# Optimization experiments

Measured on AMD Instinct MI355X. Metric: run time of the kernel, lower is better.

Reference implementation:

```python
import jax, jax.numpy as jnp
import numpy as np

# ---- static hash-grid config (matches tcnn HashGrid in __init__) ----
L = 16            # n_levels
T = 1 << 19       # hashmap size per level
BASE = 16
MAXR = 4096
GEO = 15
SCALE = np.exp((np.log(MAXR) - np.log(BASE)) / (L - 1))
RES = np.floor(BASE * SCALE ** np.arange(L)).astype(np.int64)  # per-level resolution
PRIMES = np.array([1, 2654435761, 805459861], dtype=np.uint32)
CORNERS = np.array([[(i >> 2) & 1, (i >> 1) & 1, i & 1] for i in range(8)], dtype=np.float32)  # [8,3]


@jax.custom_vjp
def trunc_exp(x):
    return jnp.exp(x)

def _te_fwd(x):
    return jnp.exp(x), x

def _te_bwd(x, g):
    return (g * jnp.exp(jnp.minimum(x, 15.0)),)

trunc_exp.defvjp(_te_fwd, _te_bwd)


def hash_encode(x, tables):
    """Multi-res hash grid. x: [N,3] in [0,1]; tables: [L,T,2] -> [N, 2*L]."""
    x = jnp.clip(x, 0.0, 1.0)
    feats = []
    for l in range(L):  # fixed small loop over levels
        res = float(RES[l])
        pos = x * res                      # [N,3]
        p0 = jnp.floor(pos)
        f = pos - p0                       # trilinear fractions
        idx = (p0[:, None, :] + CORNERS[None]).astype(jnp.uint32)  # [N,8,3]
        h = (idx[..., 0] * PRIMES[0]) ^ (idx[..., 1] * PRIMES[1]) ^ (idx[..., 2] * PRIMES[2])
        h = (h % np.uint32(T)).astype(jnp.int32)                   # [N,8]
        w = jnp.prod(jnp.where(CORNERS[None] > 0, f[:, None, :], 1.0 - f[:, None, :]), axis=-1)  # [N,8]
        feats.append(jnp.sum(tables[l][h] * w[..., None], axis=1))  # [N,2]
    return jnp.concatenate(feats, axis=-1)  # [N,32]


def sh_deg4(d):
    """Spherical harmonics degree 4 (16 comps) on unit directions d: [N,3]."""
    x, y, z = d[..., 0], d[..., 1], d[..., 2]
    x2, y2, z2 = x * x, y * y, z * z
    xy, yz, xz = x * y, y * z, x * z
    return jnp.stack([
        jnp.full_like(x, 0.28209479177387814),
        -0.48860251190291987 * y, 0.48860251190291987 * z, -0.48860251190291987 * x,
        1.0925484305920792 * xy, -1.0925484305920792 * yz,
        0.94617469575755997 * z2 - 0.31539156525252005,
        -1.0925484305920792 * xz, 0.54627421529603959 * (x2 - y2),
        -0.5900435899266435 * y * (3 * x2 - y2), 2.890611442640554 * xy * z,
        -0.4570457994644658 * y * (4 * z2 - x2 - y2),
        0.3731763325901154 * z * (2 * z2 - 3 * x2 - 3 * y2),
        -0.4570457994644658 * x * (4 * z2 - x2 - y2),
        1.445305721320277 * z * (x2 - y2),
        -0.5900435899266435 * x * (x2 - 3 * y2),
    ], axis=-1)


def setup_inputs() -> dict:
    key = jax.random.key(0)
    ks = jax.random.split(key, 12)
    R, N = 8192, 524288
    rays_o = jax.random.uniform(ks[0], (R, 3), minval=-0.4, maxval=0.4, dtype=jnp.float32)
    d = jax.random.normal(ks[1], (R, 3), dtype=jnp.float32)
    rays_d = d / jnp.linalg.norm(d, axis=-1, keepdims=True)
    ray_indices = jnp.sort(jax.random.randint(ks[2], (N,), 0, R)).astype(jnp.int32)
    t_starts = jax.random.uniform(ks[3], (N,), dtype=jnp.float32) * 0.25
    t_ends = t_starts + jax.random.uniform(ks[4], (N,), dtype=jnp.float32) * 0.02 + 1e-3
    hash_tables = jax.random.uniform(ks[5], (L, T, 2), minval=-1e-4, maxval=1e-4, dtype=jnp.float32)
    base_w0 = jax.random.normal(ks[6], (32, 64), dtype=jnp.float32) * (1.0 / np.sqrt(32))
    base_w1 = jax.random.normal(ks[7], (64, 16), dtype=jnp.float32) * (1.0 / np.sqrt(64))
    head_w0 = jax.random.normal(ks[8], (31, 64), dtype=jnp.float32) * (1.0 / np.sqrt(31))
    head_w1 = jax.random.normal(ks[9], (64, 64), dtype=jnp.float32) * (1.0 / np.sqrt(64))
    head_w2 = jax.random.normal(ks[10], (64, 3), dtype=jnp.float32) * (1.0 / np.sqrt(64))
    aabb = jnp.array([-1., -1., -1., 1., 1., 1.], dtype=jnp.float32)
    return dict(t_starts=t_starts, t_ends=t_ends, rays_o=rays_o, rays_d=rays_d,
                ray_indices=ray_indices, hash_tables=hash_tables,
                base_w0=base_w0, base_w1=base_w1,
                head_w0=head_w0, head_w1=head_w1, head_w2=head_w2, aabb=aabb)


def reference(t_starts, t_ends, rays_o, rays_d, ray_indices, hash_tables,
              base_w0, base_w1, head_w0, head_w1, head_w2, aabb):
    n_rays = rays_o.shape[0]
    aabb_min, aabb_max = aabb[:3], aabb[3:]
    # gather per-sample origins/dirs (irregular gather)
    t_origins = rays_o[ray_indices]
    t_dirs = rays_d[ray_indices]
    tmid = (t_starts + t_ends) * 0.5
    positions = t_origins + t_dirs * tmid[:, None]
    # query_density
    xn = (positions - aabb_min) / (aabb_max - aabb_min + 1e-5)
    selector = jnp.all((xn > 0.0) & (xn < 1.0), axis=-1)
    enc = hash_encode(xn, hash_tables)                   # [N,32]
    h = jax.nn.relu(enc @ base_w0) @ base_w1             # [N,16]
    sigmas = trunc_exp(h[:, 0] - 1.0) * selector         # [N]
    embedding = h[:, 1:]                                 # [N,15]
    # query_rgb: dir=(dir+1)/2 then SH enc maps back to [-1,1] => SH(t_dirs)
    hh = jnp.concatenate([sh_deg4(t_dirs), embedding], axis=-1)  # [N,31]
    rgbs = jax.nn.sigmoid(jax.nn.relu(jax.nn.relu(hh @ head_w0) @ head_w1) @ head_w2)  # [N,3]
    # render_weight_from_density: segment-wise exclusive transmittance
    s = sigmas * (t_ends - t_starts)
    excl = jnp.cumsum(s) - s                              # global exclusive cumsum
    offsets = jax.ops.segment_min(excl, ray_indices, num_segments=n_rays)  # value at each segment start
    trans = jnp.exp(-(excl - offsets[ray_indices]))
    alphas = 1.0 - jnp.exp(-s)
    weights = trans * alphas
    # accumulate_along_rays (segment_sum scatter)
    colors = jax.ops.segment_sum(weights[:, None] * rgbs, ray_indices, num_segments=n_rays)
    opacities = jax.ops.segment_sum(weights, ray_indices, num_segments=n_rays)[:, None]
    depths = jax.ops.segment_sum(weights * tmid, ray_indices, num_segments=n_rays)[:, None]
    depths = depths / jnp.maximum(opacities, jnp.finfo(jnp.float32).eps)  # expected_depths
    return colors, opacities, depths
```

## Files before the change

kernel.cpp:

```cpp
#include <hip/hip_runtime.h>
#include <math.h>

#define NLEV 16
#define TBL  (1u << 19)
#define TMASK (TBL - 1u)

typedef _Float16 half2v  __attribute__((ext_vector_type(2)));
typedef _Float16 half4   __attribute__((ext_vector_type(4)));
typedef _Float16 half8   __attribute__((ext_vector_type(8)));
typedef float    floatx4 __attribute__((ext_vector_type(4)));
typedef unsigned int uint4v __attribute__((ext_vector_type(4)));

struct ResParams { float resf[NLEV]; };

__device__ __forceinline__ float sigmoidf(float x) {
    return 1.0f / (1.0f + __expf(-x));
}

__device__ __forceinline__ int swz64(int row, int col) {
    return row * 64 + ((((col >> 3) ^ (row & 7)) << 3) | (col & 7));
}
__device__ __forceinline__ int swz64_blk(int row, int blk) {
    return row * 64 + ((blk ^ (row & 7)) << 3);
}
__device__ __forceinline__ int swz16(int row, int col) {
    return row * 64 + ((((col >> 3) ^ (row & 7)) << 3) | (col & 7));
}
__device__ __forceinline__ int swz16_blk(int row, int blk) {
    return row * 64 + ((blk ^ (row & 7)) << 3);
}

__global__ __launch_bounds__(256) void k_cvt(
    const float* __restrict__ src, _Float16* __restrict__ dst, int n4)
{
    const int i = blockIdx.x * 256 + threadIdx.x;
    if (i >= n4) return;
    const float4 v = ((const float4*)src)[i];
    half4 o; o[0] = (_Float16)v.x; o[1] = (_Float16)v.y;
    o[2] = (_Float16)v.z; o[3] = (_Float16)v.w;
    ((half4*)dst)[i] = o;
}

struct SampPos { float x0, x1, x2; };

__device__ __forceinline__ SampPos load_pos(
    int i, const float* __restrict__ t_starts, const float* __restrict__ t_ends,
    const float* __restrict__ rays_o, const float* __restrict__ rays_d,
    const int* __restrict__ ray_indices,
    float a0, float a1, float a2, float ib0, float ib1, float ib2)
{
    const int   ri = ray_indices[i];
    const float tmid = 0.5f * (t_starts[i] + t_ends[i]);
    const float xn0 = (rays_o[ri*3+0] + rays_d[ri*3+0]*tmid - a0) * ib0;
    const float xn1 = (rays_o[ri*3+1] + rays_d[ri*3+1]*tmid - a1) * ib1;
    const float xn2 = (rays_o[ri*3+2] + rays_d[ri*3+2]*tmid - a2) * ib2;
    SampPos p;
    p.x0 = fminf(fmaxf(xn0, 0.f), 1.f);
    p.x1 = fminf(fmaxf(xn1, 0.f), 1.f);
    p.x2 = fminf(fmaxf(xn2, 0.f), 1.f);
    return p;
}

__global__ __launch_bounds__(512) void k_hash2(
    const float* __restrict__ t_starts, const float* __restrict__ t_ends,
    const float* __restrict__ rays_o,   const float* __restrict__ rays_d,
    const int*   __restrict__ ray_indices,
    const _Float16* __restrict__ tabh,
    const float* __restrict__ aabb,
    _Float16* __restrict__ encG, int n, ResParams rp)
{
    const int nh = (n + 1) >> 1;
    const int iA = blockIdx.x * 512 + threadIdx.x;
    if (iA >= nh) return;
    int iB = iA + nh;
    const bool hasB = iB < n;
    if (!hasB) iB = iA;

    const float a0 = aabb[0], a1 = aabb[1], a2 = aabb[2];
    const float ib0 = 1.f / (aabb[3] - a0 + 1e-5f);
    const float ib1 = 1.f / (aabb[4] - a1 + 1e-5f);
    const float ib2 = 1.f / (aabb[5] - a2 + 1e-5f);

    const SampPos A = load_pos(iA, t_starts, t_ends, rays_o, rays_d, ray_indices,
                               a0, a1, a2, ib0, ib1, ib2);
    const SampPos B = load_pos(iB, t_starts, t_ends, rays_o, rays_d, ray_indices,
                               a0, a1, a2, ib0, ib1, ib2);

    union { _Float16 h[32]; uint4v q[4]; } evA, evB;

    #pragma unroll
    for (int l = 0; l < NLEV; ++l) {
        const float resf = rp.resf[l];
        const _Float16* __restrict__ tab = tabh + (size_t)l * (size_t)(TBL * 2u);

        const float pA0 = A.x0*resf, pA1 = A.x1*resf, pA2 = A.x2*resf;
        const float flA0 = floorf(pA0), flA1 = floorf(pA1), flA2 = floorf(pA2);
        const float fA0 = pA0-flA0, fA1 = pA1-flA1, fA2 = pA2-flA2;
        const unsigned iA0 = (unsigned)flA0, iA1 = (unsigned)flA1, iA2 = (unsigned)flA2;
        const unsigned hAx0 = iA0,               hAx1 = iA0 + 1u;
        const unsigned hAy0 = iA1 * 2654435761u, hAy1 = hAy0 + 2654435761u;
        const unsigned hAz0 = iA2 * 805459861u,  hAz1 = hAz0 + 805459861u;
        const float gA0 = 1.f-fA0, gA1 = 1.f-fA1, gA2 = 1.f-fA2;

        const float pB0 = B.x0*resf, pB1 = B.x1*resf, pB2 = B.x2*resf;
        const float flB0 = floorf(pB0), flB1 = floorf(pB1), flB2 = floorf(pB2);
        const float fB0 = pB0-flB0, fB1 = pB1-flB1, fB2 = pB2-flB2;
        const unsigned iB0 = (unsigned)flB0, iB1 = (unsigned)flB1, iB2 = (unsigned)flB2;
        const unsigned hBx0 = iB0,               hBx1 = iB0 + 1u;
        const unsigned hBy0 = iB1 * 2654435761u, hBy1 = hBy0 + 2654435761u;
        const unsigned hBz0 = iB2 * 805459861u,  hBz1 = hBz0 + 805459861u;
        const float gB0 = 1.f-fB0, gB1 = 1.f-fB1, gB2 = 1.f-fB2;

        half2v tvA[8], tvB[8];
        #pragma unroll
        for (int c = 0; c < 8; ++c) {
            const unsigned hA = (((c&4)?hAx1:hAx0) ^ ((c&2)?hAy1:hAy0)
                               ^ ((c&1)?hAz1:hAz0)) & TMASK;
            tvA[c] = *(const half2v*)(tab + (size_t)hA * 2u);
        }
        #pragma unroll
        for (int c = 0; c < 8; ++c) {
            const unsigned hB = (((c&4)?hBx1:hBx0) ^ ((c&2)?hBy1:hBy0)
                               ^ ((c&1)?hBz1:hBz0)) & TMASK;
            tvB[c] = *(const half2v*)(tab + (size_t)hB * 2u);
        }

        float eA0 = 0.f, eA1 = 0.f, eB0 = 0.f, eB1 = 0.f;
        #pragma unroll
        for (int c = 0; c < 8; ++c) {
            const float wA = (((c&4)?fA0:gA0) * ((c&2)?fA1:gA1)) * ((c&1)?fA2:gA2);
            eA0 = fmaf((float)tvA[c][0], wA, eA0);
            eA1 = fmaf((float)tvA[c][1], wA, eA1);
            const float wB = (((c&4)?fB0:gB0) * ((c&2)?fB1:gB1)) * ((c&1)?fB2:gB2);
            eB0 = fmaf((float)tvB[c][0], wB, eB0);
            eB1 = fmaf((float)tvB[c][1], wB, eB1);
        }
        evA.h[2*l]   = (_Float16)(eA0 * 1024.f);
        evA.h[2*l+1] = (_Float16)(eA1 * 1024.f);
        evB.h[2*l]   = (_Float16)(eB0 * 1024.f);
        evB.h[2*l+1] = (_Float16)(eB1 * 1024.f);
    }

    uint4v* dstA = (uint4v*)(encG + (size_t)iA * 32);
    #pragma unroll
    for (int q = 0; q < 4; ++q) __builtin_nontemporal_store(evA.q[q], dstA + q);
    if (hasB) {
        uint4v* dstB = (uint4v*)(encG + (size_t)iB * 32);
        #pragma unroll
        for (int q = 0; q < 4; ++q) __builtin_nontemporal_store(evB.q[q], dstB + q);
    }
}

__global__ __launch_bounds__(256) void k_mlp(
    const float* __restrict__ t_starts, const float* __restrict__ t_ends,
    const float* __restrict__ rays_o,   const float* __restrict__ rays_d,
    const int*   __restrict__ ray_indices,
    const float* __restrict__ bw0,
    const float* __restrict__ bw1,
    const float* __restrict__ hw0,
    const float* __restrict__ hw1,
    const float* __restrict__ hw2,
    const float* __restrict__ aabb,
    const _Float16* __restrict__ encG,
    float4* __restrict__ srgb, int n)
{
    __shared__ _Float16 sT  [4][16 * 72];
    __shared__ _Float16 sSH [256 * 16];
    __shared__ _Float16 sHB [256 * 16];
    __shared__ _Float16 sW0T[64 * 40];
    __shared__ _Float16 sW1T[64 * 64];
    __shared__ _Float16 sBW0T[64 * 32];
    __shared__ _Float16 sBW1T[16 * 64];
    __shared__ float    sHW2[192];
    __shared__ float    sDT [256];

    const int t     = threadIdx.x;
    const int gbase = blockIdx.x * 256;

    {
        const int s  = gbase + t;
        const int ri = ray_indices[s];
        const float ts = t_starts[s], te = t_ends[s];
        const float tmid = 0.5f * (ts + te);
        const float ox = rays_o[ri*3+0], oy = rays_o[ri*3+1], oz = rays_o[ri*3+2];
        const float dx = rays_d[ri*3+0], dy = rays_d[ri*3+1], dz = rays_d[ri*3+2];
        const float a0 = aabb[0], a1 = aabb[1], a2c = aabb[2];
        const float b0 = aabb[3], b1 = aabb[4], b2c = aabb[5];
        const float xn0 = (ox + dx*tmid - a0) / (b0 - a0 + 1e-5f);
        const float xn1 = (oy + dy*tmid - a1) / (b1 - a1 + 1e-5f);
        const float xn2 = (oz + dz*tmid - a2c) / (b2c - a2c + 1e-5f);
        const bool sel = (xn0 > 0.f) && (xn0 < 1.f) && (xn1 > 0.f) && (xn1 < 1.f)
                      && (xn2 > 0.f) && (xn2 < 1.f);
        sDT[t] = sel ? (te - ts) : 0.f;

        const float x = dx, y = dy, z = dz;
        const float x2 = x*x, y2 = y*y, z2 = z*z;
        const float xy = x*y, yz = y*z, xz = x*z;
        float shv[16];
        shv[0]  = 0.28209479177387814f;
        shv[1]  = -0.48860251190291987f * y;
        shv[2]  = 0.48860251190291987f * z;
        shv[3]  = -0.48860251190291987f * x;
        shv[4]  = 1.0925484305920792f * xy;
        shv[5]  = -1.0925484305920792f * yz;
        shv[6]  = 0.94617469575756f * z2 - 0.31539156525252005f;
        shv[7]  = -1.0925484305920792f * xz;
        shv[8]  = 0.5462742152960396f * (x2 - y2);
        shv[9]  = -0.5900435899266435f * y * (3.f*x2 - y2);
        shv[10] = 2.890611442640554f * xy * z;
        shv[11] = -0.4570457994644658f * y * (4.f*z2 - x2 - y2);
        shv[12] = 0.3731763325901154f * z * (2.f*z2 - 3.f*x2 - 3.f*y2);
        shv[13] = -0.4570457994644658f * x * (4.f*z2 - x2 - y2);
        shv[14] = 1.445305721320277f * z * (x2 - y2);
        shv[15] = -0.5900435899266435f * x * (x2 - 3.f*y2);
        #pragma unroll
        for (int k4 = 0; k4 < 4; ++k4) {
            half4 p;
            #pragma unroll
            for (int j = 0; j < 4; ++j) p[j] = (_Float16)shv[k4*4 + j];
            *(half4*)&sSH[t*16 + k4*4] = p;
        }
    }
    {
        const int nidx = t & 63, g = t >> 6;
        #pragma unroll
        for (int i2 = 0; i2 < 8; ++i2) {
            const int k = g*8 + i2;
            const float v = (k < 31) ? hw0[k*64 + nidx] : 0.f;
            sW0T[nidx*40 + k] = (_Float16)v;
        }
        #pragma unroll
        for (int i2 = 0; i2 < 16; ++i2) {
            const int k = g*16 + i2;
            sW1T[swz64(nidx, k)] = (_Float16)hw1[k*64 + nidx];
        }
        #pragma unroll
        for (int i2 = 0; i2 < 8; ++i2) {
            const int k = g*8 + i2;
            sBW0T[nidx*32 + k] = (_Float16)bw0[k*64 + nidx];
        }
        if (t < 192) sHW2[t] = hw2[t];
    }
    {
        const int nidx = t & 15, g = t >> 4;
        #pragma unroll
        for (int i2 = 0; i2 < 4; ++i2) {
            const int k = g*4 + i2;
            sBW1T[swz16(nidx, k)] = (_Float16)bw1[k*16 + nidx];
        }
    }

    const int lane = t & 63, w = t >> 6;
    const int nn = lane & 15, quad = lane >> 4;
    _Float16* myT = &sT[w][0];

    __syncthreads();

    const int rbase = w * 64;
    float sigv[16];

    #pragma unroll
    for (int rt = 0; rt < 4; ++rt) {
        const int srow = rbase + rt*16;
        const int drow = srow + quad*4;

        half8 bE = *(const half8*)(encG + (size_t)(gbase + srow + nn)*32 + quad*8);
        #pragma unroll
        for (int ct = 0; ct < 4; ++ct) {
            half8 aW = *(const half8*)&sBW0T[(ct*16 + nn)*32 + quad*8];
            floatx4 acc = {0.f, 0.f, 0.f, 0.f};
            acc = __builtin_amdgcn_mfma_f32_16x16x32_f16(aW, bE, acc, 0, 0, 0);
            half4 p;
            #pragma unroll
            for (int r2 = 0; r2 < 4; ++r2) p[r2] = (_Float16)fmaxf(acc[r2], 0.f);
            *(half4*)&myT[nn*72 + ct*16 + quad*4] = p;
        }

        {
            half8 a20 = *(const half8*)&myT[nn*72 +  0 + quad*8];
            half8 a21 = *(const half8*)&myT[nn*72 + 32 + quad*8];
            half8 b20 = *(const half8*)&sBW1T[swz16_blk(nn, quad)];
            half8 b21 = *(const half8*)&sBW1T[swz16_blk(nn, 4 + quad)];
            floatx4 acc = {0.f, 0.f, 0.f, 0.f};
            acc = __builtin_amdgcn_mfma_f32_16x16x32_f16(a20, b20, acc, 0, 0, 0);
            acc = __builtin_amdgcn_mfma_f32_16x16x32_f16(a21, b21, acc, 0, 0, 0);
            #pragma unroll
            for (int r2 = 0; r2 < 4; ++r2) {
                const float h = acc[r2] * (1.f / 1024.f);
                if (nn == 0) {
                    sigv[rt*4 + r2] = __expf(h - 1.f) * sDT[drow + r2];
                    sHB[(drow + r2)*16 + 15] = (_Float16)0.f;
                } else {
                    sHB[(drow + r2)*16 + (nn - 1)] = (_Float16)h;
                }
            }
        }

        half8 shf = *(const half8*)&sSH[(srow + nn)*16 + (quad & 1)*8];
        half8 hbf = *(const half8*)&sHB[(srow + nn)*16 + (quad & 1)*8];
        half8 a3f = (quad < 2) ? shf : hbf;
        #pragma unroll
        for (int ct = 0; ct < 4; ++ct) {
            half8 aW = *(const half8*)&sW0T[(ct*16 + nn)*40 + quad*8];
            floatx4 acc = {0.f, 0.f, 0.f, 0.f};
            acc = __builtin_amdgcn_mfma_f32_16x16x32_f16(aW, a3f, acc, 0, 0, 0);
            half4 p;
            #pragma unroll
            for (int r2 = 0; r2 < 4; ++r2) p[r2] = (_Float16)fmaxf(acc[r2], 0.f);
            *(half4*)&myT[nn*72 + ct*16 + quad*4] = p;
        }

        half8 af0 = *(const half8*)&myT[nn*72 +  0 + quad*8];
        half8 af1 = *(const half8*)&myT[nn*72 + 32 + quad*8];
        float pr[4][3];
        #pragma unroll
        for (int r2 = 0; r2 < 4; ++r2) { pr[r2][0]=0.f; pr[r2][1]=0.f; pr[r2][2]=0.f; }
        #pragma unroll
        for (int ct = 0; ct < 4; ++ct) {
            half8 bf0 = *(const half8*)&sW1T[swz64_blk(ct*16 + nn, quad)];
            half8 bf1 = *(const half8*)&sW1T[swz64_blk(ct*16 + nn, 4 + quad)];
            floatx4 acc = {0.f, 0.f, 0.f, 0.f};
            acc = __builtin_amdgcn_mfma_f32_16x16x32_f16(af0, bf0, acc, 0, 0, 0);
            acc = __builtin_amdgcn_mfma_f32_16x16x32_f16(af1, bf1, acc, 0, 0, 0);
            const float w0c = sHW2[(ct*16 + nn)*3 + 0];
            const float w1c = sHW2[(ct*16 + nn)*3 + 1];
            const float w2c = sHW2[(ct*16 + nn)*3 + 2];
            #pragma unroll
            for (int r2 = 0; r2 < 4; ++r2) {
                const float a3v = fmaxf(acc[r2], 0.f);
                pr[r2][0] = fmaf(a3v, w0c, pr[r2][0]);
                pr[r2][1] = fmaf(a3v, w1c, pr[r2][1]);
                pr[r2][2] = fmaf(a3v, w2c, pr[r2][2]);
            }
        }
        #pragma unroll
        for (int off = 1; off < 16; off <<= 1)
            #pragma unroll
            for (int r2 = 0; r2 < 4; ++r2) {
                pr[r2][0] += __shfl_xor(pr[r2][0], off, 64);
                pr[r2][1] += __shfl_xor(pr[r2][1], off, 64);
                pr[r2][2] += __shfl_xor(pr[r2][2], off, 64);
            }
        if (nn == 0) {
            #pragma unroll
            for (int r2 = 0; r2 < 4; ++r2) {
                float4 o;
                o.x = sigv[rt*4 + r2];
                o.y = sigmoidf(pr[r2][0]);
                o.z = sigmoidf(pr[r2][1]);
                o.w = sigmoidf(pr[r2][2]);
                srgb[gbase + drow + r2] = o;
            }
        }
    }
}

__global__ __launch_bounds__(256) void k_render(
    const float* __restrict__ t_starts, const float* __restrict__ t_ends,
    const int*   __restrict__ ray_indices,
    const float4* __restrict__ srgb,
    float* __restrict__ out, int n_samples, int n_rays)
{
    const int wid  = (blockIdx.x * 256 + threadIdx.x) >> 6;
    const int lane = threadIdx.x & 63;
    if (wid >= n_rays) return;
    const int r = wid;

    int lo = 0, hi = n_samples;
    while (lo < hi) { int mid = (lo + hi) >> 1; if (ray_indices[mid] <  r) lo = mid + 1; else hi = mid; }
    const int start = lo;
    hi = n_samples;
    while (lo < hi) { int mid = (lo + hi) >> 1; if (ray_indices[mid] <= r) lo = mid + 1; else hi = mid; }
    const int end = lo;

    float S = 0.f, cr = 0.f, cg = 0.f, cb = 0.f, op = 0.f, dw = 0.f;
    for (int j0 = start; j0 < end; j0 += 64) {
        const int j = j0 + lane;
        float s = 0.f, R = 0.f, G = 0.f, B = 0.f, tm = 0.f;
        if (j < end) {
            const float4 v = srgb[j];
            s = v.x; R = v.y; G = v.z; B = v.w;
            tm = 0.5f * (t_starts[j] + t_ends[j]);
        }
        float incl = s;
        #pragma unroll
        for (int off = 1; off < 64; off <<= 1) {
            const float tv = __shfl_up(incl, off, 64);
            if (lane >= off) incl += tv;
        }
        const float excl  = incl - s;
        const float trans = __expf(-(S + excl));
        const float alpha = 1.f - __expf(-s);
        const float wgt   = trans * alpha;
        cr += wgt * R; cg += wgt * G; cb += wgt * B;
        op += wgt;     dw += wgt * tm;
        S += __shfl(incl, 63, 64);
    }
    #pragma unroll
    for (int off = 1; off < 64; off <<= 1) {
        cr += __shfl_xor(cr, off, 64);
        cg += __shfl_xor(cg, off, 64);
        cb += __shfl_xor(cb, off, 64);
        op += __shfl_xor(op, off, 64);
        dw += __shfl_xor(dw, off, 64);
    }
    if (lane == 0) {
        out[r*3 + 0] = cr;
        out[r*3 + 1] = cg;
        out[r*3 + 2] = cb;
        out[n_rays*3 + r] = op;
        out[n_rays*4 + r] = dw / fmaxf(op, 1.1920929e-7f);
    }
}

extern "C" void kernel_launch(void* const* d_in, const int* in_sizes, int n_in,
                              void* d_out, int out_size, void* d_ws, size_t ws_size,
                              hipStream_t stream)
{
    const float* t_starts    = (const float*)d_in[0];
    const float* t_ends      = (const float*)d_in[1];
    const float* rays_o      = (const float*)d_in[2];
    const float* rays_d      = (const float*)d_in[3];
    const int*   ray_indices = (const int*)  d_in[4];
    const float* tables      = (const float*)d_in[5];
    const float* bw0         = (const float*)d_in[6];
    const float* bw1         = (const float*)d_in[7];
    const float* hw0         = (const float*)d_in[8];
    const float* hw1         = (const float*)d_in[9];
    const float* hw2         = (const float*)d_in[10];
    const float* aabb        = (const float*)d_in[11];

    const int n      = in_sizes[0];
    const int n_rays = in_sizes[2] / 3;
    const int tbl_n  = in_sizes[5];

    float* out = (float*)d_out;
    char*  ws  = (char*)d_ws;

    const size_t tabh_bytes = (size_t)tbl_n * 2;
    const size_t enc_bytes  = (size_t)n * 64;

    ResParams rp;
    const double scale = exp((log(4096.0) - log(16.0)) / 15.0);
    for (int l = 0; l < NLEV; ++l)
        rp.resf[l] = (float)floor(16.0 * pow(scale, (double)l));

    _Float16* tabh = (_Float16*)ws;
    _Float16* encG = (_Float16*)(ws + tabh_bytes);
    float4*   srgb = (float4*)(ws + tabh_bytes + enc_bytes);

    const int n4 = tbl_n / 4;
    k_cvt<<<(n4 + 255)/256, 256, 0, stream>>>(tables, tabh, n4);

    const int nh = (n + 1) >> 1;
    k_hash2<<<(nh + 511)/512, 512, 0, stream>>>(
        t_starts, t_ends, rays_o, rays_d, ray_indices, tabh, aabb, encG, n, rp);

    k_mlp<<<(n + 255)/256, 256, 0, stream>>>(
        t_starts, t_ends, rays_o, rays_d, ray_indices, bw0, bw1, hw0, hw1, hw2,
        aabb, encG, srgb, n);
    k_render<<<(n_rays*64 + 255)/256, 256, 0, stream>>>(
        t_starts, t_ends, ray_indices, srgb, out, n, n_rays);
}
```

Before: 375.7 us.

## Pair x-adjacent hash corners into 8-byte loads and run head output layer on MFMA

The hash kernel now detects when the x-floor index is even, so both x-corners hash to adjacent table entries. It then fetches them with a single 8-byte load, halving the gather count for those samples. The block size drops from 512 to 256. In the MLP kernel the last head layer (64->3) becomes an MFMA with weights padded to 16 columns, replacing per-lane FMAs and the shuffle reduction. Sigma is now broadcast by shuffle instead of being staged in a register array. The change adds branch divergence in the gather and scattered 4-byte output stores, plus some fp16 rounding of the final-layer weights.

```diff
diff --git a/kernel.cpp b/kernel.cpp
--- a/kernel.cpp
+++ b/kernel.cpp
@@ -9,12 +9,18 @@
 typedef _Float16 half4   __attribute__((ext_vector_type(4)));
 typedef _Float16 half8   __attribute__((ext_vector_type(8)));
 typedef float    floatx4 __attribute__((ext_vector_type(4)));
+typedef unsigned int uint2v __attribute__((ext_vector_type(2)));
 typedef unsigned int uint4v __attribute__((ext_vector_type(4)));
 
 struct ResParams { float resf[NLEV]; };
 
 __device__ __forceinline__ float sigmoidf(float x) {
     return 1.0f / (1.0f + __expf(-x));
+}
+
+__device__ __forceinline__ float2 unpack_h2(unsigned u) {
+    union { unsigned u; half2v h; } c; c.u = u;
+    return make_float2((float)c.h[0], (float)c.h[1]);
 }
 
 __device__ __forceinline__ int swz64(int row, int col) {
@@ -61,7 +67,31 @@
     return p;
 }
 
-__global__ __launch_bounds__(512) void k_hash2(
+__device__ __forceinline__ void corner_gather(
+    const _Float16* __restrict__ tab, unsigned i0,
+    const unsigned ryz[4], unsigned v0[4], unsigned v1[4])
+{
+    if (!(i0 & 1u)) {
+        #pragma unroll
+        for (int c = 0; c < 4; ++c) {
+            const unsigned lo = (i0 ^ ryz[c]) & TMASK;
+            const uint2v p = *(const uint2v*)(tab + (size_t)(lo & ~1u) * 2u);
+            const unsigned sw = lo & 1u;
+            v0[c] = sw ? p.y : p.x;
+            v1[c] = sw ? p.x : p.y;
+        }
+    } else {
+        #pragma unroll
+        for (int c = 0; c < 4; ++c) {
+            const unsigned lo = (i0        ^ ryz[c]) & TMASK;
+            const unsigned hi = ((i0 + 1u) ^ ryz[c]) & TMASK;
+            v0[c] = *(const unsigned*)(tab + (size_t)lo * 2u);
+            v1[c] = *(const unsigned*)(tab + (size_t)hi * 2u);
+        }
+    }
+}
+
+__global__ __launch_bounds__(256) void k_hash2(
     const float* __restrict__ t_starts, const float* __restrict__ t_ends,
     const float* __restrict__ rays_o,   const float* __restrict__ rays_d,
     const int*   __restrict__ ray_indices,
@@ -70,7 +100,7 @@
     _Float16* __restrict__ encG, int n, ResParams rp)
 {
     const int nh = (n + 1) >> 1;
-    const int iA = blockIdx.x * 512 + threadIdx.x;
+    const int iA = blockIdx.x * 256 + threadIdx.x;
     if (iA >= nh) return;
     int iB = iA + nh;
     const bool hasB = iB < n;
@@ -97,43 +127,37 @@
         const float flA0 = floorf(pA0), flA1 = floorf(pA1), flA2 = floorf(pA2);
         const float fA0 = pA0-flA0, fA1 = pA1-flA1, fA2 = pA2-flA2;
         const unsigned iA0 = (unsigned)flA0, iA1 = (unsigned)flA1, iA2 = (unsigned)flA2;
-        const unsigned hAx0 = iA0,               hAx1 = iA0 + 1u;
         const unsigned hAy0 = iA1 * 2654435761u, hAy1 = hAy0 + 2654435761u;
         const unsigned hAz0 = iA2 * 805459861u,  hAz1 = hAz0 + 805459861u;
         const float gA0 = 1.f-fA0, gA1 = 1.f-fA1, gA2 = 1.f-fA2;
+        const unsigned ryzA[4] = { hAy0^hAz0, hAy0^hAz1, hAy1^hAz0, hAy1^hAz1 };
+        const float    wyzA[4] = { gA1*gA2,   gA1*fA2,   fA1*gA2,   fA1*fA2 };
 
         const float pB0 = B.x0*resf, pB1 = B.x1*resf, pB2 = B.x2*resf;
         const float flB0 = floorf(pB0), flB1 = floorf(pB1), flB2 = floorf(pB2);
         const float fB0 = pB0-flB0, fB1 = pB1-flB1, fB2 = pB2-flB2;
         const unsigned iB0 = (unsigned)flB0, iB1 = (unsigned)flB1, iB2 = (unsigned)flB2;
-        const unsigned hBx0 = iB0,               hBx1 = iB0 + 1u;
         const unsigned hBy0 = iB1 * 2654435761u, hBy1 = hBy0 + 2654435761u;
         const unsigned hBz0 = iB2 * 805459861u,  hBz1 = hBz0 + 805459861u;
         const float gB0 = 1.f-fB0, gB1 = 1.f-fB1, gB2 = 1.f-fB2;
-
-        half2v tvA[8], tvB[8];
-        #pragma unroll
-        for (int c = 0; c < 8; ++c) {
-            const unsigned hA = (((c&4)?hAx1:hAx0) ^ ((c&2)?hAy1:hAy0)
-                               ^ ((c&1)?hAz1:hAz0)) & TMASK;
-            tvA[c] = *(const half2v*)(tab + (size_t)hA * 2u);
-        }
-        #pragma unroll
-        for (int c = 0; c < 8; ++c) {
-            const unsigned hB = (((c&4)?hBx1:hBx0) ^ ((c&2)?hBy1:hBy0)
-                               ^ ((c&1)?hBz1:hBz0)) & TMASK;
-            tvB[c] = *(const half2v*)(tab + (size_t)hB * 2u);
-        }
+        const unsigned ryzB[4] = { hBy0^hBz0, hBy0^hBz1, hBy1^hBz0, hBy1^hBz1 };
+        const float    wyzB[4] = { gB1*gB2,   gB1*fB2,   fB1*gB2,   fB1*fB2 };
+
+        unsigned vA0[4], vA1[4], vB0[4], vB1[4];
+        corner_gather(tab, iA0, ryzA, vA0, vA1);
+        corner_gather(tab, iB0, ryzB, vB0, vB1);
 
         float eA0 = 0.f, eA1 = 0.f, eB0 = 0.f, eB1 = 0.f;
         #pragma unroll
-        for (int c = 0; c < 8; ++c) {
-            const float wA = (((c&4)?fA0:gA0) * ((c&2)?fA1:gA1)) * ((c&1)?fA2:gA2);
-            eA0 = fmaf((float)tvA[c][0], wA, eA0);
-            eA1 = fmaf((float)tvA[c][1], wA, eA1);
-            const float wB = (((c&4)?fB0:gB0) * ((c&2)?fB1:gB1)) * ((c&1)?fB2:gB2);
-            eB0 = fmaf((float)tvB[c][0], wB, eB0);
-            eB1 = fmaf((float)tvB[c][1], wB, eB1);
+        for (int c = 0; c < 4; ++c) {
+            const float wAlo = gA0 * wyzA[c], wAhi = fA0 * wyzA[c];
+            const float2 ta0 = unpack_h2(vA0[c]), ta1 = unpack_h2(vA1[c]);
+            eA0 += wAlo * ta0.x + wAhi * ta1.x;
+            eA1 += wAlo * ta0.y + wAhi * ta1.y;
+            const float wBlo = gB0 * wyzB[c], wBhi = fB0 * wyzB[c];
+            const float2 tb0 = unpack_h2(vB0[c]), tb1 = unpack_h2(vB1[c]);
+            eB0 += wBlo * tb0.x + wBhi * tb1.x;
+            eB1 += wBlo * tb0.y + wBhi * tb1.y;
         }
         evA.h[2*l]   = (_Float16)(eA0 * 1024.f);
         evA.h[2*l+1] = (_Float16)(eA1 * 1024.f);
@@ -171,7 +195,6 @@
     __shared__ _Float16 sW1T[64 * 64];
     __shared__ _Float16 sBW0T[64 * 32];
     __shared__ _Float16 sBW1T[16 * 64];
-    __shared__ float    sHW2[192];
     __shared__ float    sDT [256];
 
     const int t     = threadIdx.x;
@@ -239,7 +262,6 @@
             const int k = g*8 + i2;
             sBW0T[nidx*32 + k] = (_Float16)bw0[k*64 + nidx];
         }
-        if (t < 192) sHW2[t] = hw2[t];
     }
     {
         const int nidx = t & 15, g = t >> 4;
@@ -254,10 +276,18 @@
     const int nn = lane & 15, quad = lane >> 4;
     _Float16* myT = &sT[w][0];
 
+    half8 BH2[2];
+    #pragma unroll
+    for (int ks = 0; ks < 2; ++ks)
+        #pragma unroll
+        for (int j = 0; j < 8; ++j) {
+            const int k = ks*32 + quad*8 + j;
+            BH2[ks][j] = (nn < 3) ? (_Float16)hw2[k*3 + nn] : (_Float16)0.f;
+        }
+
     __syncthreads();
 
     const int rbase = w * 64;
-    float sigv[16];
 
     #pragma unroll
     for (int rt = 0; rt < 4; ++rt) {
@@ -276,6 +306,7 @@
             *(half4*)&myT[nn*72 + ct*16 + quad*4] = p;
         }
 
+        float sigr[4];
         {
             half8 a20 = *(const half8*)&myT[nn*72 +  0 + quad*8];
             half8 a21 = *(const half8*)&myT[nn*72 + 32 + quad*8];
@@ -287,12 +318,10 @@
             #pragma unroll
             for (int r2 = 0; r2 < 4; ++r2) {
                 const float h = acc[r2] * (1.f / 1024.f);
-                if (nn == 0) {
-                    sigv[rt*4 + r2] = __expf(h - 1.f) * sDT[drow + r2];
-                    sHB[(drow + r2)*16 + 15] = (_Float16)0.f;
-                } else {
-                    sHB[(drow + r2)*16 + (nn - 1)] = (_Float16)h;
-                }
+                const float h0 = __shfl(h, lane & 0x30, 64);
+                sigr[r2] = __expf(h0 - 1.f) * sDT[drow + r2];
+                if (nn == 0) sHB[(drow + r2)*16 + 15] = (_Float16)0.f;
+                else         sHB[(drow + r2)*16 + (nn - 1)] = (_Float16)h;
             }
         }
 
@@ -312,44 +341,30 @@
 
         half8 af0 = *(const half8*)&myT[nn*72 +  0 + quad*8];
         half8 af1 = *(const half8*)&myT[nn*72 + 32 + quad*8];
-        float pr[4][3];
-        #pragma unroll
-        for (int r2 = 0; r2 < 4; ++r2) { pr[r2][0]=0.f; pr[r2][1]=0.f; pr[r2][2]=0.f; }
         #pragma unroll
         for (int ct = 0; ct < 4; ++ct) {
-            half8 bf0 = *(const half8*)&sW1T[swz64_blk(ct*16 + nn, quad)];
-            half8 bf1 = *(const half8*)&sW1T[swz64_blk(ct*16 + nn, 4 + quad)];
+            half8 aW0 = *(const half8*)&sW1T[swz64_blk(ct*16 + nn, quad)];
+            half8 aW1 = *(const half8*)&sW1T[swz64_blk(ct*16 + nn, 4 + quad)];
             floatx4 acc = {0.f, 0.f, 0.f, 0.f};
-            acc = __builtin_amdgcn_mfma_f32_16x16x32_f16(af0, bf0, acc, 0, 0, 0);
-            acc = __builtin_amdgcn_mfma_f32_16x16x32_f16(af1, bf1, acc, 0, 0, 0);
-            const float w0c = sHW2[(ct*16 + nn)*3 + 0];
-            const float w1c = sHW2[(ct*16 + nn)*3 + 1];
-            const float w2c = sHW2[(ct*16 + nn)*3 + 2];
+            acc = __builtin_amdgcn_mfma_f32_16x16x32_f16(aW0, af0, acc, 0, 0, 0);
+            acc = __builtin_amdgcn_mfma_f32_16x16x32_f16(aW1, af1, acc, 0, 0, 0);
+            half4 p;
+            #pragma unroll
+            for (int r2 = 0; r2 < 4; ++r2) p[r2] = (_Float16)fmaxf(acc[r2], 0.f);
+            *(half4*)&myT[nn*72 + ct*16 + quad*4] = p;
+        }
+
+        {
+            half8 a50 = *(const half8*)&myT[nn*72 +  0 + quad*8];
+            half8 a51 = *(const half8*)&myT[nn*72 + 32 + quad*8];
+            floatx4 acc = {0.f, 0.f, 0.f, 0.f};
+            acc = __builtin_amdgcn_mfma_f32_16x16x32_f16(a50, BH2[0], acc, 0, 0, 0);
+            acc = __builtin_amdgcn_mfma_f32_16x16x32_f16(a51, BH2[1], acc, 0, 0, 0);
             #pragma unroll
             for (int r2 = 0; r2 < 4; ++r2) {
-                const float a3v = fmaxf(acc[r2], 0.f);
-                pr[r2][0] = fmaf(a3v, w0c, pr[r2][0]);
-                pr[r2][1] = fmaf(a3v, w1c, pr[r2][1]);
-                pr[r2][2] = fmaf(a3v, w2c, pr[r2][2]);
-            }
-        }
-        #pragma unroll
-        for (int off = 1; off < 16; off <<= 1)
-            #pragma unroll
-            for (int r2 = 0; r2 < 4; ++r2) {
-                pr[r2][0] += __shfl_xor(pr[r2][0], off, 64);
-                pr[r2][1] += __shfl_xor(pr[r2][1], off, 64);
-                pr[r2][2] += __shfl_xor(pr[r2][2], off, 64);
-            }
-        if (nn == 0) {
-            #pragma unroll
-            for (int r2 = 0; r2 < 4; ++r2) {
-                float4 o;
-                o.x = sigv[rt*4 + r2];
-                o.y = sigmoidf(pr[r2][0]);
-                o.z = sigmoidf(pr[r2][1]);
-                o.w = sigmoidf(pr[r2][2]);
-                srgb[gbase + drow + r2] = o;
+                float* bp = (float*)&srgb[gbase + drow + r2];
+                if (nn < 3)       bp[1 + nn] = sigmoidf(acc[r2]);
+                else if (nn == 3) bp[0]      = sigr[r2];
             }
         }
     }
@@ -453,7 +468,7 @@
     k_cvt<<<(n4 + 255)/256, 256, 0, stream>>>(tables, tabh, n4);
 
     const int nh = (n + 1) >> 1;
-    k_hash2<<<(nh + 511)/512, 512, 0, stream>>>(
+    k_hash2<<<(nh + 255)/256, 256, 0, stream>>>(
         t_starts, t_ends, rays_o, rays_d, ray_indices, tabh, aabb, encG, n, rp);
 
     k_mlp<<<(n + 255)/256, 256, 0, stream>>>(
```

Measured after the change: 335.9 us. -10.6%, faster.
